# Optimization experiments

Hardware: AMD Instinct MI355X
Metric: run time of the kernel (lower is better)

## Reference

```python
import jax, jax.numpy as jnp
import numpy as np

B, G, I, E = 256, 24, 512, 512


def setup_inputs() -> dict:
    key = jax.random.key(0)
    k1, k2 = jax.random.split(key)
    inp = jax.random.normal(k1, (B, G, I), dtype=jnp.float32)
    weights = jax.random.normal(k2, (G, I, E), dtype=jnp.float32) * (1.0 / np.sqrt(E))
    bias = 0.1 * jnp.ones((E,), dtype=jnp.float32)
    # Cyclic group inverse-index table: row h is the permutation g -> (g - h) mod G,
    # matching symmetry_group.index2inverse_indices[h] (each row a valid permutation).
    g_ar = np.arange(G)
    inv_indices = jnp.asarray((g_ar[None, :] - g_ar[:, None]) % G, dtype=jnp.int32)
    return {"input": inp, "weights": weights, "bias": bias, "inv_indices": inv_indices}


def reference(input, weights, bias, inv_indices):
    # conv_filter[h, g, i, e] = weights[inv_indices[h, g], i, e]   -> [G, G, I, E]
    conv_filter = weights[inv_indices]
    # (input[:,None,:,:,None] * filter[None]).sum(2).sum(2) == einsum over g, i
    out = jnp.einsum("bgi,hgie->bhe", input, conv_filter)  # [B, G, E]
    return out + bias
```

## Files before the change

kernel.cpp:

```cpp
#include <hip/hip_runtime.h>
#include <hip/hip_bf16.h>
#include <stdint.h>

#define G_ 24
#define B_ 256
#define I_ 512
#define E_ 512
#define K_ (G_ * I_)

typedef __hip_bfloat16 bf16;
typedef __bf16 bf16x8 __attribute__((ext_vector_type(8)));
typedef float f32x4 __attribute__((ext_vector_type(4)));

__global__ void cvt_in_kernel(const float* __restrict__ in, bf16* __restrict__ out, int n4) {
  int idx = blockIdx.x * blockDim.x + threadIdx.x;
  if (idx >= n4) return;
  float4 v = reinterpret_cast<const float4*>(in)[idx];
  union { bf16 h[4]; uint2 u; } pk;
  pk.h[0] = __float2bfloat16(v.x);
  pk.h[1] = __float2bfloat16(v.y);
  pk.h[2] = __float2bfloat16(v.z);
  pk.h[3] = __float2bfloat16(v.w);
  reinterpret_cast<uint2*>(out)[idx] = pk.u;
}

__global__ void transpose_w_kernel(const float* __restrict__ W, bf16* __restrict__ Wt) {
  __shared__ float tile[32][33];
  const int g = blockIdx.z;
  const int i0 = blockIdx.x * 32;
  const int e0 = blockIdx.y * 32;
  const float* src = W + (size_t)g * (I_ * E_) + (size_t)(i0 + threadIdx.y) * E_ + e0 + threadIdx.x;
  #pragma unroll
  for (int r = 0; r < 32; r += 8)
    tile[threadIdx.y + r][threadIdx.x] = src[(size_t)r * E_];
  __syncthreads();
  bf16* dst = Wt + (size_t)g * (I_ * E_) + (size_t)(e0 + threadIdx.y) * I_ + i0 + threadIdx.x;
  #pragma unroll
  for (int r = 0; r < 32; r += 8)
    dst[(size_t)r * I_] = __float2bfloat16(tile[threadIdx.x][threadIdx.y + r]);
}

__global__ void init_out_kernel(const float* __restrict__ bias, float* __restrict__ out, int n4) {
  int idx = blockIdx.x * blockDim.x + threadIdx.x;
  if (idx >= n4) return;
  int e4 = idx & 127;
  reinterpret_cast<float4*>(out)[idx] = reinterpret_cast<const float4*>(bias)[e4];
}

#define FENCE() asm volatile("" ::: "memory")
#define BAR()   __builtin_amdgcn_s_barrier()
#define VMW(N)  asm volatile("s_waitcnt vmcnt(" #N ")" ::: "memory")

__device__ __forceinline__ void gload16(const bf16* g, bf16* l) {
  __builtin_amdgcn_global_load_lds((const __attribute__((address_space(1))) void*)g,
                                   (__attribute__((address_space(3))) void*)l, 16, 0, 0);
}

__global__ __launch_bounds__(256, 3) void gemm_kernel(
    const bf16* __restrict__ A,
    const bf16* __restrict__ Wt,
    float* __restrict__ out) {

  __shared__ __align__(16) bf16 ldsA[2][128 * 32];
  __shared__ __align__(16) bf16 ldsB[2][128 * 32];

  const int tid  = threadIdx.x;
  const int lane = tid & 63;
  const int wave = tid >> 6;
  const int wr   = wave >> 1;
  const int wc   = wave & 1;
  const int rsel = lane & 15;
  const int q    = lane >> 4;

  const int bid   = blockIdx.x;
  const int m0    = (bid & 1) * 128;
  const int n0    = ((bid >> 1) & 3) * 128;
  const int inner = bid >> 3;
  const int s     = inner & 3;
  const int h     = inner >> 2;

  const int c0 = tid, c1 = tid + 256;
  const size_t aoff0 = (size_t)(c0 >> 2) * K_ + (((c0 & 3) ^ ((c0 >> 3) & 3)) << 3);
  const size_t aoff1 = (size_t)(c1 >> 2) * K_ + (((c1 & 3) ^ ((c1 >> 3) & 3)) << 3);
  const size_t boff0 = (size_t)(c0 >> 2) * I_ + (((c0 & 3) ^ ((c0 >> 3) & 3)) << 3);
  const size_t boff1 = (size_t)(c1 >> 2) * I_ + (((c1 & 3) ^ ((c1 >> 3) & 3)) << 3);

  int aro[4], bro[4];
  #pragma unroll
  for (int mi = 0; mi < 4; ++mi) {
    int r = wr * 64 + mi * 16 + rsel;
    aro[mi] = r * 64 + ((q ^ ((r >> 1) & 3)) << 4);
  }
  #pragma unroll
  for (int ni = 0; ni < 4; ++ni) {
    int r = wc * 64 + ni * 16 + rsel;
    bro[ni] = r * 64 + ((q ^ ((r >> 1) & 3)) << 4);
  }

  f32x4 acc[4][4];
  #pragma unroll
  for (int i = 0; i < 4; ++i)
    #pragma unroll
    for (int j = 0; j < 4; ++j)
      acc[i][j] = (f32x4){0.f, 0.f, 0.f, 0.f};

  auto stage = [&](int t, int b) {
    const int gloc  = t >> 4;
    const int gamma = t & 15;
    int gsrc = s * 6 + gloc - h;
    if (gsrc < 0) gsrc += G_;
    if (gsrc >= G_) gsrc -= G_;
    const bf16* Ab = A + (size_t)m0 * K_ + ((size_t)s * 96 + t) * 32;
    const bf16* Bb = Wt + (size_t)gsrc * (I_ * E_) + (size_t)n0 * I_ + gamma * 32;
    gload16(Ab + aoff0, &ldsA[b][(size_t)c0 * 8]);
    gload16(Ab + aoff1, &ldsA[b][(size_t)c1 * 8]);
    gload16(Bb + boff0, &ldsB[b][(size_t)c0 * 8]);
    gload16(Bb + boff1, &ldsB[b][(size_t)c1 * 8]);
  };

#define STEP(LT, CB, NB) do {                                                    \
    if ((LT) + 1 < 96) { stage((LT) + 1, NB); VMW(4); } else { VMW(0); }         \
    FENCE(); BAR(); FENCE();                                                     \
    bf16x8 af[4], bfr[4];                                                        \
    _Pragma("unroll") for (int mi = 0; mi < 4; ++mi)                             \
      af[mi] = *(const bf16x8*)((const char*)(&ldsA[CB][0]) + aro[mi]);          \
    _Pragma("unroll") for (int ni = 0; ni < 4; ++ni)                             \
      bfr[ni] = *(const bf16x8*)((const char*)(&ldsB[CB][0]) + bro[ni]);         \
    _Pragma("unroll") for (int mi = 0; mi < 4; ++mi)                             \
      _Pragma("unroll") for (int ni = 0; ni < 4; ++ni)                           \
        acc[mi][ni] = __builtin_amdgcn_mfma_f32_16x16x32_bf16(                   \
            af[mi], bfr[ni], acc[mi][ni], 0, 0, 0);                              \
    asm volatile("s_waitcnt lgkmcnt(0)" ::: "memory");                           \
    BAR(); FENCE();                                                              \
  } while (0)

  stage(0, 0);
  for (int lt = 0; lt < 96; lt += 2) {
    STEP(lt, 0, 1);
    STEP(lt + 1, 1, 0);
  }
#undef STEP

  #pragma unroll
  for (int mi = 0; mi < 4; ++mi) {
    #pragma unroll
    for (int ni = 0; ni < 4; ++ni) {
      int ecol  = n0 + wc * 64 + ni * 16 + rsel;
      int brow0 = m0 + wr * 64 + mi * 16 + q * 4;
      float* o = out + (size_t)brow0 * (G_ * E_) + (size_t)h * E_ + ecol;
      #pragma unroll
      for (int r = 0; r < 4; ++r)
        atomicAdd(o + (size_t)r * (G_ * E_), acc[mi][ni][r]);
    }
  }
}

extern "C" void kernel_launch(void* const* d_in, const int* in_sizes, int n_in,
                              void* d_out, int out_size, void* d_ws, size_t ws_size,
                              hipStream_t stream) {
  const float* in   = (const float*)d_in[0];
  const float* w    = (const float*)d_in[1];
  const float* bias = (const float*)d_in[2];
  float* out = (float*)d_out;

  bf16* A_bf = (bf16*)d_ws;
  bf16* Wt   = (bf16*)((char*)d_ws + (size_t)B_ * K_ * 2);

  const int n4in  = (B_ * K_) / 4;
  const int n4out = (B_ * G_ * E_) / 4;
  cvt_in_kernel<<<n4in / 256, 256, 0, stream>>>(in, A_bf, n4in);
  transpose_w_kernel<<<dim3(E_ / 32, I_ / 32, G_), dim3(32, 8), 0, stream>>>(w, Wt);
  init_out_kernel<<<n4out / 256, 256, 0, stream>>>(bias, out, n4out);
  gemm_kernel<<<768, 256, 0, stream>>>(A_bf, Wt, out);
}
```

Measured before the change: 131.1 us.

## Split K five ways with uneven chunks and fuse bias init into input conversion

The GEMM's split-K factor goes from 4 to 5, with the 384 k-tiles divided into chunks of 77 and 76, so the grid grows from 768 to 960 blocks and fills the CUs more evenly. Launch bounds are raised to 4 blocks per SM. The output bias initialisation is merged into the input bf16 conversion kernel, which removes one launch because both cover the same element count. In exchange there are more atomic adds to the output, and the main loop is no longer manually unrolled by two, which may add buffer-index overhead.

```diff
diff --git a/kernel.cpp b/kernel.cpp
--- a/kernel.cpp
+++ b/kernel.cpp
@@ -12,7 +12,8 @@
 typedef __bf16 bf16x8 __attribute__((ext_vector_type(8)));
 typedef float f32x4 __attribute__((ext_vector_type(4)));
 
-__global__ void cvt_in_kernel(const float* __restrict__ in, bf16* __restrict__ out, int n4) {
+__global__ void prep_kernel(const float* __restrict__ in, bf16* __restrict__ outA,
+                            const float* __restrict__ bias, float* __restrict__ outO, int n4) {
   int idx = blockIdx.x * blockDim.x + threadIdx.x;
   if (idx >= n4) return;
   float4 v = reinterpret_cast<const float4*>(in)[idx];
@@ -21,7 +22,9 @@
   pk.h[1] = __float2bfloat16(v.y);
   pk.h[2] = __float2bfloat16(v.z);
   pk.h[3] = __float2bfloat16(v.w);
-  reinterpret_cast<uint2*>(out)[idx] = pk.u;
+  reinterpret_cast<uint2*>(outA)[idx] = pk.u;
+  int e4 = idx & 127;
+  reinterpret_cast<float4*>(outO)[idx] = reinterpret_cast<const float4*>(bias)[e4];
 }
 
 __global__ void transpose_w_kernel(const float* __restrict__ W, bf16* __restrict__ Wt) {
@@ -40,13 +43,6 @@
     dst[(size_t)r * I_] = __float2bfloat16(tile[threadIdx.x][threadIdx.y + r]);
 }
 
-__global__ void init_out_kernel(const float* __restrict__ bias, float* __restrict__ out, int n4) {
-  int idx = blockIdx.x * blockDim.x + threadIdx.x;
-  if (idx >= n4) return;
-  int e4 = idx & 127;
-  reinterpret_cast<float4*>(out)[idx] = reinterpret_cast<const float4*>(bias)[e4];
-}
-
 #define FENCE() asm volatile("" ::: "memory")
 #define BAR()   __builtin_amdgcn_s_barrier()
 #define VMW(N)  asm volatile("s_waitcnt vmcnt(" #N ")" ::: "memory")
@@ -56,7 +52,7 @@
                                    (__attribute__((address_space(3))) void*)l, 16, 0, 0);
 }
 
-__global__ __launch_bounds__(256, 3) void gemm_kernel(
+__global__ __launch_bounds__(256, 4) void gemm_kernel(
     const bf16* __restrict__ A,
     const bf16* __restrict__ Wt,
     float* __restrict__ out) {
@@ -76,8 +72,11 @@
   const int m0    = (bid & 1) * 128;
   const int n0    = ((bid >> 1) & 3) * 128;
   const int inner = bid >> 3;
-  const int s     = inner & 3;
-  const int h     = inner >> 2;
+  const int s     = inner % 5;
+  const int h     = inner / 5;
+
+  const int T0 = s * 77;
+  const int NS = (s < 4) ? 77 : 76;
 
   const int c0 = tid, c1 = tid + 256;
   const size_t aoff0 = (size_t)(c0 >> 2) * K_ + (((c0 & 3) ^ ((c0 >> 3) & 3)) << 3);
@@ -105,12 +104,10 @@
       acc[i][j] = (f32x4){0.f, 0.f, 0.f, 0.f};
 
   auto stage = [&](int t, int b) {
-    const int gloc  = t >> 4;
+    const int g     = t >> 4;
     const int gamma = t & 15;
-    int gsrc = s * 6 + gloc - h;
-    if (gsrc < 0) gsrc += G_;
-    if (gsrc >= G_) gsrc -= G_;
-    const bf16* Ab = A + (size_t)m0 * K_ + ((size_t)s * 96 + t) * 32;
+    int gsrc = g - h; if (gsrc < 0) gsrc += G_;
+    const bf16* Ab = A + (size_t)m0 * K_ + (size_t)t * 32;
     const bf16* Bb = Wt + (size_t)gsrc * (I_ * E_) + (size_t)n0 * I_ + gamma * 32;
     gload16(Ab + aoff0, &ldsA[b][(size_t)c0 * 8]);
     gload16(Ab + aoff1, &ldsA[b][(size_t)c1 * 8]);
@@ -118,28 +115,35 @@
     gload16(Bb + boff1, &ldsB[b][(size_t)c1 * 8]);
   };
 
-#define STEP(LT, CB, NB) do {                                                    \
-    if ((LT) + 1 < 96) { stage((LT) + 1, NB); VMW(4); } else { VMW(0); }         \
-    FENCE(); BAR(); FENCE();                                                     \
-    bf16x8 af[4], bfr[4];                                                        \
-    _Pragma("unroll") for (int mi = 0; mi < 4; ++mi)                             \
-      af[mi] = *(const bf16x8*)((const char*)(&ldsA[CB][0]) + aro[mi]);          \
-    _Pragma("unroll") for (int ni = 0; ni < 4; ++ni)                             \
-      bfr[ni] = *(const bf16x8*)((const char*)(&ldsB[CB][0]) + bro[ni]);         \
-    _Pragma("unroll") for (int mi = 0; mi < 4; ++mi)                             \
-      _Pragma("unroll") for (int ni = 0; ni < 4; ++ni)                           \
-        acc[mi][ni] = __builtin_amdgcn_mfma_f32_16x16x32_bf16(                   \
-            af[mi], bfr[ni], acc[mi][ni], 0, 0, 0);                              \
-    asm volatile("s_waitcnt lgkmcnt(0)" ::: "memory");                           \
-    BAR(); FENCE();                                                              \
-  } while (0)
+  stage(T0, 0);
 
-  stage(0, 0);
-  for (int lt = 0; lt < 96; lt += 2) {
-    STEP(lt, 0, 1);
-    STEP(lt + 1, 1, 0);
+  for (int lt = 0; lt < NS; ++lt) {
+    const int cur = lt & 1;
+    if (lt + 1 < NS) {
+      stage(T0 + lt + 1, cur ^ 1);
+      VMW(4);
+    } else {
+      VMW(0);
+    }
+    FENCE(); BAR(); FENCE();
+
+    bf16x8 af[4], bfr[4];
+    #pragma unroll
+    for (int mi = 0; mi < 4; ++mi)
+      af[mi] = *(const bf16x8*)((const char*)(&ldsA[cur][0]) + aro[mi]);
+    #pragma unroll
+    for (int ni = 0; ni < 4; ++ni)
+      bfr[ni] = *(const bf16x8*)((const char*)(&ldsB[cur][0]) + bro[ni]);
+    #pragma unroll
+    for (int mi = 0; mi < 4; ++mi)
+      #pragma unroll
+      for (int ni = 0; ni < 4; ++ni)
+        acc[mi][ni] = __builtin_amdgcn_mfma_f32_16x16x32_bf16(
+            af[mi], bfr[ni], acc[mi][ni], 0, 0, 0);
+
+    asm volatile("s_waitcnt lgkmcnt(0)" ::: "memory");
+    BAR(); FENCE();
   }
-#undef STEP
 
   #pragma unroll
   for (int mi = 0; mi < 4; ++mi) {
@@ -166,10 +170,8 @@
   bf16* A_bf = (bf16*)d_ws;
   bf16* Wt   = (bf16*)((char*)d_ws + (size_t)B_ * K_ * 2);
 
-  const int n4in  = (B_ * K_) / 4;
-  const int n4out = (B_ * G_ * E_) / 4;
-  cvt_in_kernel<<<n4in / 256, 256, 0, stream>>>(in, A_bf, n4in);
+  const int n4 = (B_ * K_) / 4;
+  prep_kernel<<<n4 / 256, 256, 0, stream>>>(in, A_bf, bias, out, n4);
   transpose_w_kernel<<<dim3(E_ / 32, I_ / 32, G_), dim3(32, 8), 0, stream>>>(w, Wt);
-  init_out_kernel<<<n4out / 256, 256, 0, stream>>>(bias, out, n4out);
-  gemm_kernel<<<768, 256, 0, stream>>>(A_bf, Wt, out);
+  gemm_kernel<<<960, 256, 0, stream>>>(A_bf, Wt, out);
 }
```

Measured after the change: 137.8 us. +5.1%, slower.
